# Kernel tuning notes

Measured on AMD Instinct MI355X. Metric: run time of the kernel, lower is better.

The kernel has to match this reference:

```python
import jax, jax.numpy as jnp
import numpy as np

B, C, S, HEADS, MLP = 8, 128, 32, 8, 512
EPS = 1e-5
SCALE = (C // HEADS) ** -0.5  # dim_head=16 -> 16**-0.5


def setup_inputs() -> dict:
    key = jax.random.key(0)
    ks = jax.random.split(key, 6)
    x = jax.random.normal(ks[0], (B, C, S, S, S), jnp.float32)
    qkv_w = jax.random.normal(ks[1], (3 * C, C), jnp.float32) * 0.02   # Conv3d 1x1x1, no bias
    proj_w = jax.random.normal(ks[2], (C, C), jnp.float32) * 0.02
    proj_b = jnp.zeros((C,), jnp.float32)
    ln1_w = jnp.ones((C, S, S, S), jnp.float32)
    ln1_b = jnp.zeros((C, S, S, S), jnp.float32)
    ln2_w = jnp.ones((C, S, S, S), jnp.float32)
    ln2_b = jnp.zeros((C, S, S, S), jnp.float32)
    mlp_w1 = jax.random.normal(ks[3], (MLP, C), jnp.float32) * 0.02
    mlp_b1 = jnp.zeros((MLP,), jnp.float32)
    mlp_w2 = jax.random.normal(ks[4], (C, MLP), jnp.float32) * 0.02
    mlp_b2 = jnp.zeros((C,), jnp.float32)
    return dict(x=x, qkv_w=qkv_w, proj_w=proj_w, proj_b=proj_b,
                ln1_w=ln1_w, ln1_b=ln1_b, ln2_w=ln2_w, ln2_b=ln2_b,
                mlp_w1=mlp_w1, mlp_b1=mlp_b1, mlp_w2=mlp_w2, mlp_b2=mlp_b2)


def _layernorm_full(x, w, b):
    # LayerNorm over (channel, D, H, W) per batch element, biased variance, eps=1e-5
    mu = jnp.mean(x, axis=(1, 2, 3, 4), keepdims=True)
    var = jnp.mean(jnp.square(x - mu), axis=(1, 2, 3, 4), keepdims=True)
    return (x - mu) * jax.lax.rsqrt(var + EPS) * w[None] + b[None]


def _block(x, qkv_w, proj_w, proj_b, ln1_w, ln1_b, ln2_w, ln2_b,
           mlp_w1, mlp_b1, mlp_w2, mlp_b2):
    b, c, d, h, w = x.shape
    n = d * h * w
    ch = c // HEADS
    xf = x.reshape(b, c, n)
    # 1x1x1 conv == per-voxel matmul over channels
    qkv = jnp.einsum('bcn,oc->bon', xf, qkv_w)                 # [b, 3c, n]
    q, k, v = jnp.split(qkv, 3, axis=1)
    q = q.reshape(b, HEADS, ch, n)
    k = k.reshape(b, HEADS, ch, n)
    v = v.reshape(b, HEADS, ch, n)
    # channel-channel attention: contraction over spatial tokens n
    attn = jax.nn.softmax(jnp.einsum('bhin,bhjn->bhij', q, k) * SCALE, axis=-1)
    out = jnp.einsum('bhij,bhjn->bhin', attn, v).reshape(b, c, n)
    out = jnp.einsum('bcn,oc->bon', out, proj_w) + proj_b[None, :, None]
    x1 = _layernorm_full(x + out.reshape(b, c, d, h, w), ln1_w, ln1_b)
    # MLP: conv1x1 -> exact GELU -> conv1x1
    x1f = x1.reshape(b, c, n)
    hid = jax.nn.gelu(jnp.einsum('bcn,oc->bon', x1f, mlp_w1) + mlp_b1[None, :, None],
                      approximate=False)
    m = jnp.einsum('bon,co->bcn', hid, mlp_w2) + mlp_b2[None, :, None]
    return _layernorm_full(x1 + m.reshape(b, c, d, h, w), ln2_w, ln2_b)


def reference(x, qkv_w, proj_w, proj_b, ln1_w, ln1_b, ln2_w, ln2_b,
              mlp_w1, mlp_b1, mlp_w2, mlp_b2):
    return _block(x, qkv_w, proj_w, proj_b, ln1_w, ln1_b, ln2_w, ln2_b,
                  mlp_w1, mlp_b1, mlp_w2, mlp_b2)
```

## Files before the change

### kernel.cpp

```cpp
#include <hip/hip_runtime.h>
#include <hip/hip_bf16.h>
#include <math.h>


#define N_SP 32768
typedef __hip_bfloat16 bf16;
static const size_t DS = (size_t)128 * N_SP;

typedef __attribute__((ext_vector_type(8))) short s8b;
typedef __attribute__((ext_vector_type(4))) float f4;
typedef __attribute__((ext_vector_type(4))) uint u4v;
typedef __attribute__((ext_vector_type(4))) ushort us4v;

__device__ __forceinline__ ushort f2b(float f) {
    __hip_bfloat16 h = __float2bfloat16(f);
    return *reinterpret_cast<ushort*>(&h);
}
__device__ __forceinline__ float b2f(ushort u) {
    unsigned v = ((unsigned)u) << 16;
    float f;
    __builtin_memcpy(&f, &v, 4);
    return f;
}
__device__ __forceinline__ float gelu_f(float h) {
    float u = 1.5957691216057308f * h * fmaf(0.044715f, h * h, 1.0f);
    float e = __expf(u);
    return h * (1.0f - __builtin_amdgcn_rcpf(e + 1.0f));
}
__device__ __forceinline__ int swz8(int n, int c0) {
    return n * 128 + (c0 ^ ((n & 15) << 3));
}
__device__ __forceinline__ int swz4(int n, int c0) {
    return n * 128 + (((c0 & 0x78) ^ ((n & 15) << 3)) | (c0 & 4));
}

__global__ __launch_bounds__(256) void k_transpose(const float* __restrict__ in,
                                                   float* __restrict__ out,
                                                   int R, int Ccols) {
    int idx = blockIdx.x * 256 + threadIdx.x;
    if (idx >= R * Ccols) return;
    int r = idx / Ccols, c = idx % Ccols;
    out[c * R + r] = in[idx];
}

__global__ __launch_bounds__(256) void k_cvt(const float* __restrict__ in,
                                             ushort* __restrict__ out, int n) {
    int i = blockIdx.x * 256 + threadIdx.x;
    if (i < n) out[i] = f2b(in[i]);
}

__global__ __launch_bounds__(256) void k_packln(const float* __restrict__ w,
                                                const float* __restrict__ b,
                                                uint* __restrict__ out) {
    int tid = blockIdx.x * 256 + threadIdx.x;
    int c = tid >> 15, n = tid & 32767;
    uint lo = f2b(w[tid]);
    uint hi = f2b(b[tid]);
    out[(size_t)n * 128 + c] = lo | (hi << 16);
}

__global__ __launch_bounds__(256) void k_packflat(const float* __restrict__ w,
                                                  const float* __restrict__ b,
                                                  uint* __restrict__ out) {
    int tid = blockIdx.x * 256 + threadIdx.x;
    uint lo = f2b(w[tid]);
    uint hi = f2b(b[tid]);
    out[tid] = lo | (hi << 16);
}

__global__ __launch_bounds__(256, 4) void k_cov(const float* __restrict__ x,
                                                float* __restrict__ Gpart) {
    __shared__ ushort xs[128 * 136];
    const int kb = blockIdx.x, b = blockIdx.y;
    const int t = threadIdx.x;
    const int wave = t >> 6, lane = t & 63, q = lane >> 4, r = lane & 15;
    f4 acc[8][2];
#pragma unroll
    for (int m = 0; m < 8; ++m) { acc[m][0] = (f4){0,0,0,0}; acc[m][1] = (f4){0,0,0,0}; }
    for (int ch = 0; ch < 4; ++ch) {
        const int nbase = kb * 512 + ch * 128;
        __syncthreads();
        {
            const int nq = t & 31, cr = t >> 5;
            const float* xp = x + (size_t)b * DS + nbase + nq * 4;
#pragma unroll
            for (int half = 0; half < 2; ++half) {
                f4 xv[8];
#pragma unroll
                for (int cc = 0; cc < 8; ++cc)
                    xv[cc] = __builtin_nontemporal_load(
                        (const f4*)(xp + (size_t)(cr * 16 + half * 8 + cc) * N_SP));
#pragma unroll
                for (int cc = 0; cc < 8; ++cc) {
                    int c = cr * 16 + half * 8 + cc;
                    ushort4 pk;
                    pk.x = f2b(xv[cc].x); pk.y = f2b(xv[cc].y);
                    pk.z = f2b(xv[cc].z); pk.w = f2b(xv[cc].w);
                    *(ushort4*)&xs[c * 136 + nq * 4] = pk;
                }
            }
        }
        __syncthreads();
        for (int kk = 0; kk < 4; ++kk) {
            const int c0 = kk * 32 + q * 8;
            s8b bj0 = *(const s8b*)&xs[(wave * 32 + r) * 136 + c0];
            s8b bj1 = *(const s8b*)&xs[(wave * 32 + 16 + r) * 136 + c0];
#pragma unroll
            for (int m = 0; m < 8; ++m) {
                s8b a = *(const s8b*)&xs[(m * 16 + r) * 136 + c0];
                acc[m][0] = __builtin_amdgcn_mfma_f32_16x16x32_bf16(a, bj0, acc[m][0], 0, 0, 0);
                acc[m][1] = __builtin_amdgcn_mfma_f32_16x16x32_bf16(a, bj1, acc[m][1], 0, 0, 0);
            }
        }
    }
    float* gp = Gpart + ((size_t)b * 64 + kb) * 16384;
#pragma unroll
    for (int n2 = 0; n2 < 2; ++n2)
#pragma unroll
        for (int m = 0; m < 8; ++m)
#pragma unroll
            for (int rg = 0; rg < 4; ++rg) {
                int i = m * 16 + q * 4 + rg;
                int j = wave * 32 + n2 * 16 + r;
                gp[i * 128 + j] = acc[m][n2][rg];
            }
}

__global__ __launch_bounds__(256) void k_greduce(const float* __restrict__ Gpart,
                                                 float* __restrict__ G) {
    int tid = blockIdx.x * 256 + threadIdx.x;
    int b = tid >> 14, ij = tid & 16383;
    float s = 0.f;
#pragma unroll 8
    for (int kb = 0; kb < 64; ++kb)
        s += __builtin_nontemporal_load(&Gpart[((size_t)b * 64 + kb) * 16384 + ij]);
    G[tid] = s;
}

__global__ __launch_bounds__(256) void k_gram_small(const float* __restrict__ G,
                                                    const float* __restrict__ qkv_w,
                                                    float* __restrict__ attn) {
    __shared__ float t1[16 * 132];
    __shared__ float sg[16 * 16];
    const int bh = blockIdx.x;
    const int b = bh >> 3, h = bh & 7;
    const int t = threadIdx.x;
    {
        const int i = t >> 4, c20 = (t & 15) * 8;
        const float* wq = qkv_w + (size_t)(h * 16 + i) * 128;
        const float* Gb = G + (size_t)b * 16384;
        float a[8];
#pragma unroll
        for (int k = 0; k < 8; ++k) a[k] = 0.f;
        for (int c = 0; c < 128; ++c) {
            float w = wq[c];
            const float* grow = Gb + c * 128 + c20;
#pragma unroll
            for (int k = 0; k < 8; ++k) a[k] = fmaf(w, grow[k], a[k]);
        }
#pragma unroll
        for (int k = 0; k < 8; ++k) t1[i * 132 + c20 + k] = a[k];
    }
    __syncthreads();
    {
        const int i = t >> 4, j = t & 15;
        const float* wk = qkv_w + (size_t)(128 + h * 16 + j) * 128;
        float s = 0.f;
        for (int c2 = 0; c2 < 128; ++c2) s = fmaf(t1[i * 132 + c2], wk[c2], s);
        sg[i * 16 + j] = s * 0.25f;
    }
    __syncthreads();
    if (t < 16) {
        float mx = -1e30f;
#pragma unroll
        for (int j = 0; j < 16; ++j) mx = fmaxf(mx, sg[t * 16 + j]);
        float e[16], sum = 0.f;
#pragma unroll
        for (int j = 0; j < 16; ++j) { e[j] = expf(sg[t * 16 + j] - mx); sum += e[j]; }
        float inv = 1.0f / sum;
#pragma unroll
        for (int j = 0; j < 16; ++j)
            attn[((size_t)bh * 16 + t) * 16 + j] = e[j] * inv;
    }
}

__global__ __launch_bounds__(256, 2) void k_mfold(const float* __restrict__ attn,
                                                  const float* __restrict__ qkv_w,
                                                  const float* __restrict__ PT,
                                                  ushort* __restrict__ Mbb) {
    __shared__ float t2[128 * 128];
    const int b = blockIdx.x, t = threadIdx.x;
    {
        const int hi = t >> 1, c0 = (t & 1) * 64;
        const int h = hi >> 4;
        const float* at = attn + ((size_t)b * 128 + hi) * 16;
        float a[16];
#pragma unroll
        for (int j = 0; j < 16; ++j) a[j] = at[j];
        float sc[64];
#pragma unroll
        for (int c = 0; c < 64; ++c) sc[c] = 0.f;
        for (int j = 0; j < 16; ++j) {
            const float* wv = qkv_w + (size_t)(256 + h * 16 + j) * 128 + c0;
            float aj = a[j];
#pragma unroll
            for (int c = 0; c < 64; ++c) sc[c] = fmaf(aj, wv[c], sc[c]);
        }
#pragma unroll
        for (int c = 0; c < 64; ++c) t2[hi * 128 + c0 + c] = sc[c];
    }
    __syncthreads();
    const int c = t & 127, half = t >> 7;
    float acc[128];
#pragma unroll
    for (int o = 0; o < 128; ++o) acc[o] = 0.f;
    for (int ci = half * 64; ci < half * 64 + 64; ++ci) {
        float s = t2[ci * 128 + c];
        const float* pt = PT + ci * 128;
#pragma unroll
        for (int o = 0; o < 128; ++o) acc[o] = fmaf(pt[o], s, acc[o]);
    }
    __syncthreads();
    if (half) {
#pragma unroll
        for (int o = 0; o < 128; ++o) t2[c * 128 + o] = acc[o];
    }
    __syncthreads();
    if (!half) {
        ushort* m = Mbb + (size_t)b * 16384;
#pragma unroll
        for (int o = 0; o < 128; ++o)
            m[(size_t)o * 128 + c] = f2b(acc[o] + t2[c * 128 + o]);
    }
}

__global__ __launch_bounds__(256, 3) void k_attnproj(const float* __restrict__ x,
                                                     const ushort* __restrict__ Mbb,
                                                     const float* __restrict__ proj_b,
                                                     ushort* __restrict__ x1Tb,
                                                     float* __restrict__ st) {
    __shared__ ushort xT[128 * 136];
    const int b = blockIdx.y;
    const int n0 = blockIdx.x * 128;
    const int t = threadIdx.x;
    const int wave = t >> 6, lane = t & 63, q = lane >> 4, r = lane & 15;
    {
        const int nq = (t & 31) * 4;
        const int cg = (t >> 5) * 4;
        const float* xb = x + (size_t)b * DS + n0 + nq;
#pragma unroll
        for (int ph = 0; ph < 2; ++ph) {
            f4 xv[8];
#pragma unroll
            for (int u = 0; u < 8; ++u) {
                int c = ph * 64 + cg + (u >> 2) * 32 + (u & 3);
                xv[u] = __builtin_nontemporal_load((const f4*)(xb + (size_t)c * N_SP));
            }
#pragma unroll
            for (int u2 = 0; u2 < 2; ++u2) {
                int c0 = ph * 64 + cg + u2 * 32;
#pragma unroll
                for (int i = 0; i < 4; ++i) {
                    us4v pk = { f2b(xv[u2 * 4 + 0][i]), f2b(xv[u2 * 4 + 1][i]),
                                f2b(xv[u2 * 4 + 2][i]), f2b(xv[u2 * 4 + 3][i]) };
                    *(us4v*)&xT[(nq + i) * 136 + c0] = pk;
                }
            }
        }
    }
    const int orow = wave * 32 + r;
    s8b a[8];
    {
        const ushort* mp = Mbb + (size_t)b * 16384 + (size_t)orow * 128 + q * 8;
#pragma unroll
        for (int m = 0; m < 2; ++m)
#pragma unroll
            for (int kk = 0; kk < 4; ++kk)
                a[m * 4 + kk] = *(const s8b*)(mp + m * 16 * 128 + kk * 32);
    }
    __syncthreads();
    f4 acc[2][8];
#pragma unroll
    for (int m = 0; m < 2; ++m)
#pragma unroll
        for (int j = 0; j < 8; ++j) acc[m][j] = (f4){0,0,0,0};
#pragma unroll
    for (int kk = 0; kk < 4; ++kk) {
        const int c0 = kk * 32 + q * 8;
#pragma unroll
        for (int j = 0; j < 8; ++j) {
            s8b bx = *(const s8b*)&xT[(j * 16 + r) * 136 + c0];
            acc[0][j] = __builtin_amdgcn_mfma_f32_16x16x32_bf16(a[kk],     bx, acc[0][j], 0, 0, 0);
            acc[1][j] = __builtin_amdgcn_mfma_f32_16x16x32_bf16(a[4 + kk], bx, acc[1][j], 0, 0, 0);
        }
    }
    float s = 0.f, sq = 0.f;
    float4 pbq0 = *(const float4*)&proj_b[wave * 32 + q * 4];
    float4 pbq1 = *(const float4*)&proj_b[wave * 32 + 16 + q * 4];
#pragma unroll
    for (int m = 0; m < 2; ++m) {
        const int o0 = wave * 32 + m * 16 + q * 4;
        const float4 pb = m ? pbq1 : pbq0;
#pragma unroll
        for (int j = 0; j < 8; ++j) {
            const int nn = j * 16 + r;
            ushort4 xr = *(const ushort4*)&xT[nn * 136 + o0];
            float v0 = acc[m][j][0] + pb.x + b2f(xr.x);
            float v1 = acc[m][j][1] + pb.y + b2f(xr.y);
            float v2 = acc[m][j][2] + pb.z + b2f(xr.z);
            float v3 = acc[m][j][3] + pb.w + b2f(xr.w);
            us4v ov = { f2b(v0), f2b(v1), f2b(v2), f2b(v3) };
            __builtin_nontemporal_store(ov,
                (us4v*)(x1Tb + (size_t)b * DS + (size_t)(n0 + nn) * 128 + o0));
            s += (v0 + v1) + (v2 + v3);
            sq = fmaf(v0, v0, sq); sq = fmaf(v1, v1, sq);
            sq = fmaf(v2, v2, sq); sq = fmaf(v3, v3, sq);
        }
    }
#pragma unroll
    for (int off = 32; off > 0; off >>= 1) {
        s += __shfl_down(s, off, 64);
        sq += __shfl_down(sq, off, 64);
    }
    if (lane == 0) {
        atomicAdd(&st[0 + b], s);
        atomicAdd(&st[8 + b], sq);
    }
}

__global__ void k_finalize(float* st, int off) {
    int b = threadIdx.x;
    if (b < 8) {
        const float invn = 1.0f / 4194304.0f;
        float mu = st[off + b] * invn;
        float var = st[off + 8 + b] * invn - mu * mu;
        st[off + 16 + b] = mu;
        st[off + 24 + b] = rsqrtf(var + 1e-5f);
    }
}

__global__ __launch_bounds__(256) void k_lnapply(const float* __restrict__ in,
                                                 const uint* __restrict__ lnwb,
                                                 const float* __restrict__ st, int off,
                                                 float* __restrict__ out) {
    size_t i4 = (size_t)blockIdx.x * 256 + threadIdx.x;
    int b = (int)(i4 >> 20);
    size_t cn = i4 * 4 - (size_t)b * 4194304;
    float mu = st[off + 16 + b], rs = st[off + 24 + b];
    const float4 xv = *(const float4*)(in + (size_t)b * DS + cn);
    const uint4 wv = *(const uint4*)(lnwb + cn);
    float4 o;
    o.x = fmaf((xv.x - mu) * rs, b2f((ushort)(wv.x & 0xffffu)), b2f((ushort)(wv.x >> 16)));
    o.y = fmaf((xv.y - mu) * rs, b2f((ushort)(wv.y & 0xffffu)), b2f((ushort)(wv.y >> 16)));
    o.z = fmaf((xv.z - mu) * rs, b2f((ushort)(wv.z & 0xffffu)), b2f((ushort)(wv.z >> 16)));
    o.w = fmaf((xv.w - mu) * rs, b2f((ushort)(wv.w & 0xffffu)), b2f((ushort)(wv.w >> 16)));
    *(float4*)(out + (size_t)b * DS + cn) = o;
}

__global__ __launch_bounds__(256, 2) void k_mlp(const ushort* __restrict__ x1Tb,
                                                float* __restrict__ xout,
                                                const ushort* __restrict__ w1b,
                                                const float* __restrict__ b1v,
                                                const ushort* __restrict__ w2b,
                                                const float* __restrict__ b2v,
                                                const uint* __restrict__ lnwbT,
                                                float* __restrict__ st) {
    __shared__ ushort xT[128 * 128];
    __shared__ ushort hT[128 * 128];
    const int b = blockIdx.y;
    const int n0 = blockIdx.x * 128;
    const int t = threadIdx.x;
    const int wave = t >> 6, lane = t & 63, q = lane >> 4, r = lane & 15;
    const float mu = st[16 + b], rs = st[24 + b];
    {
        const int c8 = (t & 15) * 8, rb = t >> 4;
        const ushort* xb = x1Tb + (size_t)b * DS + (size_t)n0 * 128;
        const uint*  wb = lnwbT + (size_t)n0 * 128;
#pragma unroll
        for (int gb = 0; gb < 2; ++gb) {
            s8b xv[4]; u4v wv0[4], wv1[4];
#pragma unroll
            for (int u = 0; u < 4; ++u) {
                int nn = (gb * 4 + u) * 16 + rb;
                xv[u]  = __builtin_nontemporal_load((const s8b*)(xb + (size_t)nn * 128 + c8));
                wv0[u] = __builtin_nontemporal_load((const u4v*)(wb + (size_t)nn * 128 + c8));
                wv1[u] = __builtin_nontemporal_load((const u4v*)(wb + (size_t)nn * 128 + c8 + 4));
            }
#pragma unroll
            for (int u = 0; u < 4; ++u) {
                int nn = (gb * 4 + u) * 16 + rb;
                ushort4 p0, p1;
                float xe;
                xe = b2f((ushort)xv[u][0]);
                p0.x = f2b(fmaf((xe - mu) * rs, b2f((ushort)(wv0[u].x & 0xffffu)), b2f((ushort)(wv0[u].x >> 16))));
                xe = b2f((ushort)xv[u][1]);
                p0.y = f2b(fmaf((xe - mu) * rs, b2f((ushort)(wv0[u].y & 0xffffu)), b2f((ushort)(wv0[u].y >> 16))));
                xe = b2f((ushort)xv[u][2]);
                p0.z = f2b(fmaf((xe - mu) * rs, b2f((ushort)(wv0[u].z & 0xffffu)), b2f((ushort)(wv0[u].z >> 16))));
                xe = b2f((ushort)xv[u][3]);
                p0.w = f2b(fmaf((xe - mu) * rs, b2f((ushort)(wv0[u].w & 0xffffu)), b2f((ushort)(wv0[u].w >> 16))));
                xe = b2f((ushort)xv[u][4]);
                p1.x = f2b(fmaf((xe - mu) * rs, b2f((ushort)(wv1[u].x & 0xffffu)), b2f((ushort)(wv1[u].x >> 16))));
                xe = b2f((ushort)xv[u][5]);
                p1.y = f2b(fmaf((xe - mu) * rs, b2f((ushort)(wv1[u].y & 0xffffu)), b2f((ushort)(wv1[u].y >> 16))));
                xe = b2f((ushort)xv[u][6]);
                p1.z = f2b(fmaf((xe - mu) * rs, b2f((ushort)(wv1[u].z & 0xffffu)), b2f((ushort)(wv1[u].z >> 16))));
                xe = b2f((ushort)xv[u][7]);
                p1.w = f2b(fmaf((xe - mu) * rs, b2f((ushort)(wv1[u].w & 0xffffu)), b2f((ushort)(wv1[u].w >> 16))));
                *(ushort4*)&xT[swz4(nn, c8)] = p0;
                *(ushort4*)&xT[swz4(nn, c8 + 4)] = p1;
            }
        }
    }
    const int orow = wave * 32 + r;
    s8b a1[8];
    {
        const ushort* w1p = w1b + (size_t)orow * 128 + q * 8;
#pragma unroll
        for (int m = 0; m < 2; ++m)
#pragma unroll
            for (int kk = 0; kk < 4; ++kk)
                a1[m * 4 + kk] = *(const s8b*)(w1p + m * 16 * 128 + kk * 32);
    }
    __syncthreads();
    float4 b2q0 = *(const float4*)&b2v[wave * 32 + q * 4];
    float4 b2q1 = *(const float4*)&b2v[wave * 32 + 16 + q * 4];
    f4 acc2[2][8];
#pragma unroll
    for (int j = 0; j < 8; ++j) {
        acc2[0][j] = (f4){b2q0.x, b2q0.y, b2q0.z, b2q0.w};
        acc2[1][j] = (f4){b2q1.x, b2q1.y, b2q1.z, b2q1.w};
    }

    for (int os = 0; os < 4; ++os) {
        float4 b1q0 = *(const float4*)&b1v[os * 128 + wave * 32 + q * 4];
        float4 b1q1 = *(const float4*)&b1v[os * 128 + wave * 32 + 16 + q * 4];
        f4 acc1[2][8];
#pragma unroll
        for (int j = 0; j < 8; ++j) {
            acc1[0][j] = (f4){b1q0.x, b1q0.y, b1q0.z, b1q0.w};
            acc1[1][j] = (f4){b1q1.x, b1q1.y, b1q1.z, b1q1.w};
        }
#pragma unroll
        for (int kk = 0; kk < 4; ++kk) {
            const int c0 = kk * 32 + q * 8;
#pragma unroll
            for (int j = 0; j < 8; ++j) {
                s8b bx = *(const s8b*)&xT[swz8(j * 16 + r, c0)];
                acc1[0][j] = __builtin_amdgcn_mfma_f32_16x16x32_bf16(a1[kk],     bx, acc1[0][j], 0, 0, 0);
                acc1[1][j] = __builtin_amdgcn_mfma_f32_16x16x32_bf16(a1[4 + kk], bx, acc1[1][j], 0, 0, 0);
            }
        }
        s8b a2[8];
        {
            const ushort* w2p = w2b + (size_t)orow * 512 + os * 128 + q * 8;
#pragma unroll
            for (int m = 0; m < 2; ++m)
#pragma unroll
                for (int kk = 0; kk < 4; ++kk)
                    a2[m * 4 + kk] = *(const s8b*)(w2p + m * 16 * 512 + kk * 32);
        }
#pragma unroll
        for (int m = 0; m < 2; ++m) {
            const int hr0 = wave * 32 + m * 16 + q * 4;
#pragma unroll
            for (int j = 0; j < 8; ++j) {
                ushort4 pk;
                pk.x = f2b(gelu_f(acc1[m][j][0]));
                pk.y = f2b(gelu_f(acc1[m][j][1]));
                pk.z = f2b(gelu_f(acc1[m][j][2]));
                pk.w = f2b(gelu_f(acc1[m][j][3]));
                *(ushort4*)&hT[swz4(j * 16 + r, hr0)] = pk;
            }
        }
        __syncthreads();
#pragma unroll
        for (int kk = 0; kk < 4; ++kk) {
            const int c0 = kk * 32 + q * 8;
#pragma unroll
            for (int j = 0; j < 8; ++j) {
                s8b hx = *(const s8b*)&hT[swz8(j * 16 + r, c0)];
                acc2[0][j] = __builtin_amdgcn_mfma_f32_16x16x32_bf16(a2[kk],     hx, acc2[0][j], 0, 0, 0);
                acc2[1][j] = __builtin_amdgcn_mfma_f32_16x16x32_bf16(a2[4 + kk], hx, acc2[1][j], 0, 0, 0);
            }
        }
        if (os < 3) {
            const ushort* w1p = w1b + (size_t)((os + 1) * 128 + orow) * 128 + q * 8;
#pragma unroll
            for (int m = 0; m < 2; ++m)
#pragma unroll
                for (int kk = 0; kk < 4; ++kk)
                    a1[m * 4 + kk] = *(const s8b*)(w1p + m * 16 * 128 + kk * 32);
        }
        __syncthreads();
    }
    float s = 0.f, sq = 0.f;
#pragma unroll
    for (int m = 0; m < 2; ++m) {
        const int o0 = wave * 32 + m * 16 + q * 4;
#pragma unroll
        for (int j = 0; j < 8; ++j) {
            const int nn = j * 16 + r;
            ushort4 xr = *(const ushort4*)&xT[swz4(nn, o0)];
            float v0 = acc2[m][j][0] + b2f(xr.x);
            float v1 = acc2[m][j][1] + b2f(xr.y);
            float v2 = acc2[m][j][2] + b2f(xr.z);
            float v3 = acc2[m][j][3] + b2f(xr.w);
            float* op = xout + (size_t)b * DS + n0 + nn;
            __builtin_nontemporal_store(v0, op + (size_t)(o0 + 0) * N_SP);
            __builtin_nontemporal_store(v1, op + (size_t)(o0 + 1) * N_SP);
            __builtin_nontemporal_store(v2, op + (size_t)(o0 + 2) * N_SP);
            __builtin_nontemporal_store(v3, op + (size_t)(o0 + 3) * N_SP);
            s += (v0 + v1) + (v2 + v3);
            sq = fmaf(v0, v0, sq); sq = fmaf(v1, v1, sq);
            sq = fmaf(v2, v2, sq); sq = fmaf(v3, v3, sq);
        }
    }
#pragma unroll
    for (int off = 32; off > 0; off >>= 1) {
        s += __shfl_down(s, off, 64);
        sq += __shfl_down(sq, off, 64);
    }
    if (lane == 0) {
        atomicAdd(&st[32 + b], s);
        atomicAdd(&st[40 + b], sq);
    }
}

extern "C" void kernel_launch(void* const* d_in, const int* in_sizes, int n_in,
                              void* d_out, int out_size, void* d_ws, size_t ws_size,
                              hipStream_t stream) {
    const float* x      = (const float*)d_in[0];
    const float* qkv_w  = (const float*)d_in[1];
    const float* proj_w = (const float*)d_in[2];
    const float* proj_b = (const float*)d_in[3];
    const float* ln1_w  = (const float*)d_in[4];
    const float* ln1_b  = (const float*)d_in[5];
    const float* ln2_w  = (const float*)d_in[6];
    const float* ln2_b  = (const float*)d_in[7];
    const float* mlp_w1 = (const float*)d_in[8];
    const float* mlp_b1 = (const float*)d_in[9];
    const float* mlp_w2 = (const float*)d_in[10];
    const float* mlp_b2 = (const float*)d_in[11];
    float* out = (float*)d_out;

    char* wsb = (char*)d_ws;
    float*  st    = (float*)wsb;
    float*  attn  = (float*)(wsb + 256);
    float*  PT    = (float*)(wsb + 65792);
    ushort* Mbb   = (ushort*)(wsb + 131328);
    ushort* w1b   = (ushort*)(wsb + 393472);
    ushort* w2b   = (ushort*)(wsb + 524544);
    float*  G     = (float*)(wsb + 655616);
    uint*   lnwbT = (uint*)(wsb + 1179904);
    float*  Gpart = (float*)(wsb + 18874368);
    ushort* x1Tb  = (ushort*)(wsb + 18874368);
    uint*   lnwb2 = (uint*)(wsb + 18874368);

    hipMemsetAsync(st, 0, 64 * sizeof(float), stream);

    k_transpose<<<64, 256, 0, stream>>>(proj_w, PT, 128, 128);
    k_cvt<<<256, 256, 0, stream>>>(mlp_w1, w1b, 65536);
    k_cvt<<<256, 256, 0, stream>>>(mlp_w2, w2b, 65536);
    k_packln<<<16384, 256, 0, stream>>>(ln1_w, ln1_b, lnwbT);

    k_cov<<<dim3(64, 8), 256, 0, stream>>>(x, Gpart);
    k_greduce<<<512, 256, 0, stream>>>(Gpart, G);
    k_gram_small<<<64, 256, 0, stream>>>(G, qkv_w, attn);
    k_mfold<<<8, 256, 0, stream>>>(attn, qkv_w, PT, Mbb);

    k_attnproj<<<dim3(256, 8), 256, 0, stream>>>(x, Mbb, proj_b, x1Tb, st);
    k_finalize<<<1, 64, 0, stream>>>(st, 0);
    k_mlp<<<dim3(256, 8), 256, 0, stream>>>(x1Tb, out, w1b, mlp_b1, w2b, mlp_b2,
                                            lnwbT, st);
    k_packflat<<<16384, 256, 0, stream>>>(ln2_w, ln2_b, lnwb2);
    k_finalize<<<1, 64, 0, stream>>>(st, 32);
    k_lnapply<<<32768, 256, 0, stream>>>(out, lnwb2, st, 32, out);
}
```

Before: 953.3 us.

## Tile LN1 weight pack transpose, drop LN2 pack, and tune output store patterns

The LN1 weight/bias packing kernel now does its transpose through an LDS tile, giving coalesced reads and vectorised writes instead of scattered 4-byte stores. The LN2 packing kernel is removed, and the final layernorm reads fp32 weight and bias directly, which avoids writing and re-reading a packed buffer. The MLP output stores switch from nontemporal to normal stores, possibly so the final layernorm can hit them in cache, and the attention-projection epilogue loop order is swapped. The trade-off is that the final layernorm now reads more bytes per element from two fp32 arrays.

```diff
diff --git a/kernel.cpp b/kernel.cpp
--- a/kernel.cpp
+++ b/kernel.cpp
@@ -52,20 +52,30 @@
 __global__ __launch_bounds__(256) void k_packln(const float* __restrict__ w,
                                                 const float* __restrict__ b,
                                                 uint* __restrict__ out) {
-    int tid = blockIdx.x * 256 + threadIdx.x;
-    int c = tid >> 15, n = tid & 32767;
-    uint lo = f2b(w[tid]);
-    uint hi = f2b(b[tid]);
-    out[(size_t)n * 128 + c] = lo | (hi << 16);
-}
-
-__global__ __launch_bounds__(256) void k_packflat(const float* __restrict__ w,
-                                                  const float* __restrict__ b,
-                                                  uint* __restrict__ out) {
-    int tid = blockIdx.x * 256 + threadIdx.x;
-    uint lo = f2b(w[tid]);
-    uint hi = f2b(b[tid]);
-    out[tid] = lo | (hi << 16);
+    __shared__ uint tile[64 * 128];
+    const int n0 = blockIdx.x * 64;
+    const int t = threadIdx.x;
+    {
+        const int c = t >> 1, nh = (t & 1) * 32;
+        const float* wp = w + (size_t)c * N_SP + n0 + nh;
+        const float* bp = b + (size_t)c * N_SP + n0 + nh;
+#pragma unroll
+        for (int g = 0; g < 8; ++g) {
+            f4 wv = __builtin_nontemporal_load((const f4*)(wp + g * 4));
+            f4 bv = __builtin_nontemporal_load((const f4*)(bp + g * 4));
+            tile[(nh + g * 4 + 0) * 128 + c] = (uint)f2b(wv.x) | ((uint)f2b(bv.x) << 16);
+            tile[(nh + g * 4 + 1) * 128 + c] = (uint)f2b(wv.y) | ((uint)f2b(bv.y) << 16);
+            tile[(nh + g * 4 + 2) * 128 + c] = (uint)f2b(wv.z) | ((uint)f2b(bv.z) << 16);
+            tile[(nh + g * 4 + 3) * 128 + c] = (uint)f2b(wv.w) | ((uint)f2b(bv.w) << 16);
+        }
+    }
+    __syncthreads();
+    uint* op = out + (size_t)n0 * 128;
+#pragma unroll
+    for (int g = 0; g < 8; ++g) {
+        int idx = g * 256 + t;
+        *(uint4*)(op + idx * 4) = *(const uint4*)&tile[idx * 4];
+    }
 }
 
 __global__ __launch_bounds__(256, 4) void k_cov(const float* __restrict__ x,
@@ -298,20 +308,20 @@
     float4 pbq0 = *(const float4*)&proj_b[wave * 32 + q * 4];
     float4 pbq1 = *(const float4*)&proj_b[wave * 32 + 16 + q * 4];
 #pragma unroll
-    for (int m = 0; m < 2; ++m) {
-        const int o0 = wave * 32 + m * 16 + q * 4;
-        const float4 pb = m ? pbq1 : pbq0;
-#pragma unroll
-        for (int j = 0; j < 8; ++j) {
-            const int nn = j * 16 + r;
+    for (int j = 0; j < 8; ++j) {
+        const int nn = j * 16 + r;
+        ushort* obase = x1Tb + (size_t)b * DS + (size_t)(n0 + nn) * 128;
+#pragma unroll
+        for (int m = 0; m < 2; ++m) {
+            const int o0 = wave * 32 + m * 16 + q * 4;
+            const float4 pb = m ? pbq1 : pbq0;
             ushort4 xr = *(const ushort4*)&xT[nn * 136 + o0];
             float v0 = acc[m][j][0] + pb.x + b2f(xr.x);
             float v1 = acc[m][j][1] + pb.y + b2f(xr.y);
             float v2 = acc[m][j][2] + pb.z + b2f(xr.z);
             float v3 = acc[m][j][3] + pb.w + b2f(xr.w);
             us4v ov = { f2b(v0), f2b(v1), f2b(v2), f2b(v3) };
-            __builtin_nontemporal_store(ov,
-                (us4v*)(x1Tb + (size_t)b * DS + (size_t)(n0 + nn) * 128 + o0));
+            __builtin_nontemporal_store(ov, (us4v*)(obase + o0));
             s += (v0 + v1) + (v2 + v3);
             sq = fmaf(v0, v0, sq); sq = fmaf(v1, v1, sq);
             sq = fmaf(v2, v2, sq); sq = fmaf(v3, v3, sq);
@@ -340,7 +350,8 @@
 }
 
 __global__ __launch_bounds__(256) void k_lnapply(const float* __restrict__ in,
-                                                 const uint* __restrict__ lnwb,
+                                                 const float* __restrict__ lnw,
+                                                 const float* __restrict__ lnb,
                                                  const float* __restrict__ st, int off,
                                                  float* __restrict__ out) {
     size_t i4 = (size_t)blockIdx.x * 256 + threadIdx.x;
@@ -348,12 +359,13 @@
     size_t cn = i4 * 4 - (size_t)b * 4194304;
     float mu = st[off + 16 + b], rs = st[off + 24 + b];
     const float4 xv = *(const float4*)(in + (size_t)b * DS + cn);
-    const uint4 wv = *(const uint4*)(lnwb + cn);
+    const float4 wv = *(const float4*)(lnw + cn);
+    const float4 bv = *(const float4*)(lnb + cn);
     float4 o;
-    o.x = fmaf((xv.x - mu) * rs, b2f((ushort)(wv.x & 0xffffu)), b2f((ushort)(wv.x >> 16)));
-    o.y = fmaf((xv.y - mu) * rs, b2f((ushort)(wv.y & 0xffffu)), b2f((ushort)(wv.y >> 16)));
-    o.z = fmaf((xv.z - mu) * rs, b2f((ushort)(wv.z & 0xffffu)), b2f((ushort)(wv.z >> 16)));
-    o.w = fmaf((xv.w - mu) * rs, b2f((ushort)(wv.w & 0xffffu)), b2f((ushort)(wv.w >> 16)));
+    o.x = fmaf((xv.x - mu) * rs, wv.x, bv.x);
+    o.y = fmaf((xv.y - mu) * rs, wv.y, bv.y);
+    o.z = fmaf((xv.z - mu) * rs, wv.z, bv.z);
+    o.w = fmaf((xv.w - mu) * rs, wv.w, bv.w);
     *(float4*)(out + (size_t)b * DS + cn) = o;
 }
 
@@ -507,10 +519,10 @@
             float v2 = acc2[m][j][2] + b2f(xr.z);
             float v3 = acc2[m][j][3] + b2f(xr.w);
             float* op = xout + (size_t)b * DS + n0 + nn;
-            __builtin_nontemporal_store(v0, op + (size_t)(o0 + 0) * N_SP);
-            __builtin_nontemporal_store(v1, op + (size_t)(o0 + 1) * N_SP);
-            __builtin_nontemporal_store(v2, op + (size_t)(o0 + 2) * N_SP);
-            __builtin_nontemporal_store(v3, op + (size_t)(o0 + 3) * N_SP);
+            op[(size_t)(o0 + 0) * N_SP] = v0;
+            op[(size_t)(o0 + 1) * N_SP] = v1;
+            op[(size_t)(o0 + 2) * N_SP] = v2;
+            op[(size_t)(o0 + 3) * N_SP] = v3;
             s += (v0 + v1) + (v2 + v3);
             sq = fmaf(v0, v0, sq); sq = fmaf(v1, v1, sq);
             sq = fmaf(v2, v2, sq); sq = fmaf(v3, v3, sq);
@@ -555,14 +567,13 @@
     uint*   lnwbT = (uint*)(wsb + 1179904);
     float*  Gpart = (float*)(wsb + 18874368);
     ushort* x1Tb  = (ushort*)(wsb + 18874368);
-    uint*   lnwb2 = (uint*)(wsb + 18874368);
 
     hipMemsetAsync(st, 0, 64 * sizeof(float), stream);
 
     k_transpose<<<64, 256, 0, stream>>>(proj_w, PT, 128, 128);
     k_cvt<<<256, 256, 0, stream>>>(mlp_w1, w1b, 65536);
     k_cvt<<<256, 256, 0, stream>>>(mlp_w2, w2b, 65536);
-    k_packln<<<16384, 256, 0, stream>>>(ln1_w, ln1_b, lnwbT);
+    k_packln<<<512, 256, 0, stream>>>(ln1_w, ln1_b, lnwbT);
 
     k_cov<<<dim3(64, 8), 256, 0, stream>>>(x, Gpart);
     k_greduce<<<512, 256, 0, stream>>>(Gpart, G);
@@ -573,7 +584,6 @@
     k_finalize<<<1, 64, 0, stream>>>(st, 0);
     k_mlp<<<dim3(256, 8), 256, 0, stream>>>(x1Tb, out, w1b, mlp_b1, w2b, mlp_b2,
                                             lnwbT, st);
-    k_packflat<<<16384, 256, 0, stream>>>(ln2_w, ln2_b, lnwb2);
     k_finalize<<<1, 64, 0, stream>>>(st, 32);
-    k_lnapply<<<32768, 256, 0, stream>>>(out, lnwb2, st, 32, out);
-}
+    k_lnapply<<<32768, 256, 0, stream>>>(out, ln2_w, ln2_b, st, 32, out);
+}
```

Result: no change. 958.2 us (+0.5%).
